# Optimization experiments

Measured on AMD Instinct MI355X. Metric: run time of the kernel, lower is better.

The kernel has to match this reference:

```python
import jax, jax.numpy as jnp
import numpy as np

B, T, N_EMBD, HEAD_SIZE = 64, 512, 384, 64


def setup_inputs() -> dict:
    key = jax.random.key(0)
    k1, k2, k3, k4 = jax.random.split(key, 4)
    x = jax.random.normal(k1, (B, T, N_EMBD), dtype=jnp.float32)
    scale = 1.0 / np.sqrt(N_EMBD)
    Wq = jax.random.normal(k2, (N_EMBD, HEAD_SIZE), dtype=jnp.float32) * scale
    Wk = jax.random.normal(k3, (N_EMBD, HEAD_SIZE), dtype=jnp.float32) * scale
    Wv = jax.random.normal(k4, (N_EMBD, HEAD_SIZE), dtype=jnp.float32) * scale
    return {"x": x, "Wq": Wq, "Wk": Wk, "Wv": Wv}


def reference(x, Wq, Wk, Wv):
    # Single-head causal self-attention (dropout = identity / eval mode).
    q = jnp.einsum('btc,ch->bth', x, Wq)  # [B,T,H]
    k = jnp.einsum('btc,ch->bth', x, Wk)
    v = jnp.einsum('btc,ch->bth', x, Wv)
    scale = q.shape[-1] ** -0.5
    scores = jnp.einsum('bth,bsh->bts', q, k) * scale  # [B,T,T]
    Tlen = x.shape[1]
    causal = jnp.tril(jnp.ones((Tlen, Tlen), dtype=bool))
    scores = jnp.where(causal, scores, -jnp.inf)
    weights = jax.nn.softmax(scores, axis=-1)
    out = jnp.einsum('bts,bsh->bth', weights, v)  # [B,T,H]
    return out
```

## Files before the change

kernel.cpp:

```cpp
#include <hip/hip_runtime.h>


typedef __bf16 bf16_t;
typedef __bf16 bf16x8 __attribute__((ext_vector_type(8)));
typedef __bf16 bf16x4 __attribute__((ext_vector_type(4)));
typedef float  f32x4  __attribute__((ext_vector_type(4)));

__device__ __forceinline__ bf16x8 ld_b128(const bf16_t* p) {
    return *reinterpret_cast<const bf16x8*>(p);
}

__device__ __forceinline__ void async_copy16(void* lds, const void* g) {
    __builtin_amdgcn_global_load_lds(
        (const __attribute__((address_space(1))) unsigned int*)g,
        (__attribute__((address_space(3))) unsigned int*)lds,
        16, 0, 0);
}

__global__ __launch_bounds__(256) void wt_kernel(const float* __restrict__ Wq,
                                                 const float* __restrict__ Wk,
                                                 const float* __restrict__ Wv,
                                                 bf16_t* __restrict__ Wt) {
    int idx = blockIdx.x * 256 + threadIdx.x;
    int p = idx / (384 * 64);
    int r = idx - p * (384 * 64);
    int c = r >> 6;
    int h = r & 63;
    const float* W = (p == 0) ? Wq : (p == 1) ? Wk : Wv;
    Wt[p * 24576 + h * 384 + c] = (bf16_t)W[c * 64 + h];
}

__global__ __launch_bounds__(256, 2) void qkv_kernel(const float* __restrict__ x,
                                                     const bf16_t* __restrict__ Wt,
                                                     bf16_t* __restrict__ Q,
                                                     bf16_t* __restrict__ K,
                                                     bf16_t* __restrict__ Vt) {
    const int tid  = threadIdx.x;
    const int wave = tid >> 6, lane = tid & 63;
    const int quad = lane >> 4, l16 = lane & 15;
    const int rowbase = blockIdx.x * 64;
    const int batch   = rowbase >> 9;

    __shared__ alignas(16) bf16_t xs[64][392];

    bf16x8 Bf[3][12];
    #pragma unroll
    for (int nt = 0; nt < 3; ++nt) {
        int col  = wave * 48 + nt * 16 + l16;
        int proj = col >> 6, h = col & 63;
        const bf16_t* wp = Wt + proj * 24576 + h * 384 + quad * 8;
        #pragma unroll
        for (int kk = 0; kk < 12; ++kk) Bf[nt][kk] = ld_b128(wp + kk * 32);
    }

    #pragma unroll
    for (int i = 0; i < 12; ++i) {
        int idx = i * 256 + tid;
        int row = idx / 48;
        int p   = idx - row * 48;
        const float* src = x + (rowbase + row) * 384 + p * 8;
        float4 a = *reinterpret_cast<const float4*>(src);
        float4 c = *reinterpret_cast<const float4*>(src + 4);
        bf16x8 v = {(bf16_t)a.x, (bf16_t)a.y, (bf16_t)a.z, (bf16_t)a.w,
                    (bf16_t)c.x, (bf16_t)c.y, (bf16_t)c.z, (bf16_t)c.w};
        *reinterpret_cast<bf16x8*>(&xs[row][p * 8]) = v;
    }
    __syncthreads();

    #pragma unroll
    for (int rt = 0; rt < 4; ++rt) {
        f32x4 acc[3];
        #pragma unroll
        for (int nt = 0; nt < 3; ++nt) acc[nt] = (f32x4){0.f, 0.f, 0.f, 0.f};

        #pragma unroll
        for (int kk = 0; kk < 12; ++kk) {
            bf16x8 a = *reinterpret_cast<const bf16x8*>(&xs[rt * 16 + l16][kk * 32 + quad * 8]);
            #pragma unroll
            for (int nt = 0; nt < 3; ++nt)
                acc[nt] = __builtin_amdgcn_mfma_f32_16x16x32_bf16(a, Bf[nt][kk], acc[nt], 0, 0, 0);
        }

        #pragma unroll
        for (int nt = 0; nt < 3; ++nt) {
            int col  = wave * 48 + nt * 16 + l16;
            int proj = col >> 6, h = col & 63;
            int trow = rowbase + rt * 16 + quad * 4;
            if (proj == 0) {
                #pragma unroll
                for (int r = 0; r < 4; ++r) Q[(trow + r) * 64 + h] = (bf16_t)acc[nt][r];
            } else if (proj == 1) {
                #pragma unroll
                for (int r = 0; r < 4; ++r) K[(trow + r) * 64 + h] = (bf16_t)acc[nt][r];
            } else {
                bf16x4 v = {(bf16_t)acc[nt][0], (bf16_t)acc[nt][1],
                            (bf16_t)acc[nt][2], (bf16_t)acc[nt][3]};
                *reinterpret_cast<bf16x4*>(Vt + batch * 32768 + h * 512 + (trow & 511)) = v;
            }
        }
    }
}

__global__ __launch_bounds__(256, 2) void attn_kernel(const bf16_t* __restrict__ Q,
                                                      const bf16_t* __restrict__ K,
                                                      const bf16_t* __restrict__ Vt,
                                                      float* __restrict__ out) {
    const int tid  = threadIdx.x;
    const int wave = tid >> 6, lane = tid & 63;
    const int quad = lane >> 4, l16 = lane & 15;
    const int b    = blockIdx.x >> 3;
    const int j    = blockIdx.x & 7;
    const int rbase = j * 64 + wave * 16;
    const int rowq  = rbase + quad * 4;

    __shared__ alignas(16) bf16_t Kt[2][64 * 64];
    __shared__ alignas(16) bf16_t Vtt[2][64 * 64];
    __shared__ alignas(16) bf16_t Pl[4][16 * 64];

    const bf16_t* Kb = K  + b * 32768;
    const bf16_t* Vb = Vt + b * 32768;

    const bf16_t* qptr = Q + (b * 512 + rbase + l16) * 64 + quad * 8;
    bf16x8 aq0 = ld_b128(qptr);
    bf16x8 aq1 = ld_b128(qptr + 32);

    f32x4 acc_o[4];
    #pragma unroll
    for (int nt = 0; nt < 4; ++nt) acc_o[nt] = (f32x4){0.f, 0.f, 0.f, 0.f};
    float l_lane[4] = {0.f, 0.f, 0.f, 0.f};

    auto stage = [&](int buf, int kb) {
        #pragma unroll
        for (int i = 0; i < 2; ++i) {
            int rr = wave * 16 + i * 8 + (lane >> 3);
            int g  = (lane & 7) ^ (rr & 7);
            async_copy16(&Kt[buf][(wave * 16 + i * 8) * 64],
                         Kb + (kb + rr) * 64 + g * 8);
            async_copy16(&Vtt[buf][(wave * 16 + i * 8) * 64],
                         Vb + rr * 512 + kb + g * 8);
        }
    };

    stage(0, 0);
    for (int kt = 0; kt <= j; ++kt) {
        int buf = kt & 1;
        __syncthreads();
        if (kt < j) stage(1 - buf, (kt + 1) * 64);
        int kb = kt * 64;
        bool last = (kt == j);

        float s[4][4];
        #pragma unroll
        for (int nt = 0; nt < 4; ++nt) {
            int tk = nt * 16 + l16;
            f32x4 c = (f32x4){0.f, 0.f, 0.f, 0.f};
            bf16x8 bk0 = ld_b128(&Kt[buf][tk * 64 + (((0 + quad) ^ (tk & 7)) << 3)]);
            c = __builtin_amdgcn_mfma_f32_16x16x32_bf16(aq0, bk0, c, 0, 0, 0);
            bf16x8 bk1 = ld_b128(&Kt[buf][tk * 64 + (((4 + quad) ^ (tk & 7)) << 3)]);
            c = __builtin_amdgcn_mfma_f32_16x16x32_bf16(aq1, bk1, c, 0, 0, 0);
            #pragma unroll
            for (int r = 0; r < 4; ++r) s[nt][r] = c[r];
        }
        if (last) {
            #pragma unroll
            for (int nt = 0; nt < 4; ++nt)
                #pragma unroll
                for (int r = 0; r < 4; ++r)
                    if (kb + nt * 16 + l16 > rowq + r) s[nt][r] = -__builtin_inff();
        }

        bf16_t* pw = &Pl[wave][0];
        #pragma unroll
        for (int nt = 0; nt < 4; ++nt) {
            #pragma unroll
            for (int r = 0; r < 4; ++r) {
                float p = __expf(fmaf(s[nt][r], 0.125f, -20.0f));
                l_lane[r] += p;
                int rl  = quad * 4 + r;
                int col = nt * 16 + l16;
                pw[rl * 64 + (((col >> 3) ^ (rl & 7)) << 3) + (col & 7)] = (bf16_t)p;
            }
        }
        bf16x8 ap0 = ld_b128(&pw[l16 * 64 + (((0 + quad) ^ (l16 & 7)) << 3)]);
        bf16x8 ap1 = ld_b128(&pw[l16 * 64 + (((4 + quad) ^ (l16 & 7)) << 3)]);
        #pragma unroll
        for (int nth = 0; nth < 4; ++nth) {
            int h = nth * 16 + l16;
            bf16x8 bv0 = ld_b128(&Vtt[buf][h * 64 + (((0 + quad) ^ (h & 7)) << 3)]);
            acc_o[nth] = __builtin_amdgcn_mfma_f32_16x16x32_bf16(ap0, bv0, acc_o[nth], 0, 0, 0);
            bf16x8 bv1 = ld_b128(&Vtt[buf][h * 64 + (((4 + quad) ^ (h & 7)) << 3)]);
            acc_o[nth] = __builtin_amdgcn_mfma_f32_16x16x32_bf16(ap1, bv1, acc_o[nth], 0, 0, 0);
        }
    }

    #pragma unroll
    for (int r = 0; r < 4; ++r) {
        float l = l_lane[r];
        #pragma unroll
        for (int xm = 1; xm < 16; xm <<= 1) l += __shfl_xor(l, xm, 64);
        l_lane[r] = l;
    }

    #pragma unroll
    for (int nth = 0; nth < 4; ++nth) {
        #pragma unroll
        for (int r = 0; r < 4; ++r) {
            out[(b * 512 + rowq + r) * 64 + nth * 16 + l16] =
                acc_o[nth][r] / l_lane[r];
        }
    }
}

extern "C" void kernel_launch(void* const* d_in, const int* in_sizes, int n_in,
                              void* d_out, int out_size, void* d_ws, size_t ws_size,
                              hipStream_t stream) {
    const float* x  = (const float*)d_in[0];
    const float* Wq = (const float*)d_in[1];
    const float* Wk = (const float*)d_in[2];
    const float* Wv = (const float*)d_in[3];

    char* ws = (char*)d_ws;
    bf16_t* Wt = (bf16_t*)(ws);
    bf16_t* Q  = (bf16_t*)(ws + 147456);
    bf16_t* K  = (bf16_t*)(ws + 147456 + 4194304);
    bf16_t* Vt = (bf16_t*)(ws + 147456 + 8388608);

    wt_kernel<<<dim3(288), dim3(256), 0, stream>>>(Wq, Wk, Wv, Wt);
    qkv_kernel<<<dim3(512), dim3(256), 0, stream>>>(x, Wt, Q, K, Vt);
    attn_kernel<<<dim3(512), dim3(256), 0, stream>>>(Q, K, Vt, (float*)d_out);
}
```

Before: 115.0 us.

## Double-buffer x tiles via async global-to-LDS loads in QKV projection

```diff
diff --git a/kernel.cpp b/kernel.cpp
--- a/kernel.cpp
+++ b/kernel.cpp
@@ -41,7 +41,7 @@
     const int rowbase = blockIdx.x * 64;
     const int batch   = rowbase >> 9;
 
-    __shared__ alignas(16) bf16_t xs[64][392];
+    __shared__ alignas(16) float xs[2][64 * 128];
 
     bf16x8 Bf[3][12];
     #pragma unroll
@@ -53,34 +53,52 @@
         for (int kk = 0; kk < 12; ++kk) Bf[nt][kk] = ld_b128(wp + kk * 32);
     }
 
-    #pragma unroll
-    for (int i = 0; i < 12; ++i) {
-        int idx = i * 256 + tid;
-        int row = idx / 48;
-        int p   = idx - row * 48;
-        const float* src = x + (rowbase + row) * 384 + p * 8;
-        float4 a = *reinterpret_cast<const float4*>(src);
-        float4 c = *reinterpret_cast<const float4*>(src + 4);
-        bf16x8 v = {(bf16_t)a.x, (bf16_t)a.y, (bf16_t)a.z, (bf16_t)a.w,
-                    (bf16_t)c.x, (bf16_t)c.y, (bf16_t)c.z, (bf16_t)c.w};
-        *reinterpret_cast<bf16x8*>(&xs[row][p * 8]) = v;
-    }
-    __syncthreads();
+    auto stage = [&](int buf, int c) {
+        const float* src = x + rowbase * 384 + c * 128;
+        #pragma unroll
+        for (int i = 0; i < 8; ++i) {
+            int g   = wave * 512 + i * 64 + lane;
+            int row = g >> 5, gc = g & 31;
+            int gs  = (gc & 24) | ((gc ^ row) & 7);
+            async_copy16(&xs[buf][(wave * 512 + i * 64) * 4],
+                         src + row * 384 + gs * 4);
+        }
+    };
+
+    f32x4 acc[4][3];
+    #pragma unroll
+    for (int rt = 0; rt < 4; ++rt)
+        #pragma unroll
+        for (int nt = 0; nt < 3; ++nt) acc[rt][nt] = (f32x4){0.f, 0.f, 0.f, 0.f};
+
+    stage(0, 0);
+    for (int c = 0; c < 3; ++c) {
+        int buf = c & 1;
+        __syncthreads();
+        if (c < 2) stage(1 - buf, c + 1);
+        #pragma unroll
+        for (int rt = 0; rt < 4; ++rt) {
+            int row = rt * 16 + l16;
+            const float* xr = &xs[buf][row * 128];
+            #pragma unroll
+            for (int kk = 0; kk < 4; ++kk) {
+                int G0 = kk * 8 + quad * 2;
+                int g0 = (G0 & 24) | ((G0 ^ row) & 7);
+                int g1 = ((G0 + 1) & 24) | (((G0 + 1) ^ row) & 7);
+                f32x4 a0 = *reinterpret_cast<const f32x4*>(xr + g0 * 4);
+                f32x4 a1 = *reinterpret_cast<const f32x4*>(xr + g1 * 4);
+                bf16x8 a = {(bf16_t)a0[0], (bf16_t)a0[1], (bf16_t)a0[2], (bf16_t)a0[3],
+                            (bf16_t)a1[0], (bf16_t)a1[1], (bf16_t)a1[2], (bf16_t)a1[3]};
+                #pragma unroll
+                for (int nt = 0; nt < 3; ++nt)
+                    acc[rt][nt] = __builtin_amdgcn_mfma_f32_16x16x32_bf16(
+                        a, Bf[nt][c * 4 + kk], acc[rt][nt], 0, 0, 0);
+            }
+        }
+    }
 
     #pragma unroll
     for (int rt = 0; rt < 4; ++rt) {
-        f32x4 acc[3];
-        #pragma unroll
-        for (int nt = 0; nt < 3; ++nt) acc[nt] = (f32x4){0.f, 0.f, 0.f, 0.f};
-
-        #pragma unroll
-        for (int kk = 0; kk < 12; ++kk) {
-            bf16x8 a = *reinterpret_cast<const bf16x8*>(&xs[rt * 16 + l16][kk * 32 + quad * 8]);
-            #pragma unroll
-            for (int nt = 0; nt < 3; ++nt)
-                acc[nt] = __builtin_amdgcn_mfma_f32_16x16x32_bf16(a, Bf[nt][kk], acc[nt], 0, 0, 0);
-        }
-
         #pragma unroll
         for (int nt = 0; nt < 3; ++nt) {
             int col  = wave * 48 + nt * 16 + l16;
@@ -88,13 +106,13 @@
             int trow = rowbase + rt * 16 + quad * 4;
             if (proj == 0) {
                 #pragma unroll
-                for (int r = 0; r < 4; ++r) Q[(trow + r) * 64 + h] = (bf16_t)acc[nt][r];
+                for (int r = 0; r < 4; ++r) Q[(trow + r) * 64 + h] = (bf16_t)acc[rt][nt][r];
             } else if (proj == 1) {
                 #pragma unroll
-                for (int r = 0; r < 4; ++r) K[(trow + r) * 64 + h] = (bf16_t)acc[nt][r];
+                for (int r = 0; r < 4; ++r) K[(trow + r) * 64 + h] = (bf16_t)acc[rt][nt][r];
             } else {
-                bf16x4 v = {(bf16_t)acc[nt][0], (bf16_t)acc[nt][1],
-                            (bf16_t)acc[nt][2], (bf16_t)acc[nt][3]};
+                bf16x4 v = {(bf16_t)acc[rt][nt][0], (bf16_t)acc[rt][nt][1],
+                            (bf16_t)acc[rt][nt][2], (bf16_t)acc[rt][nt][3]};
                 *reinterpret_cast<bf16x4*>(Vt + batch * 32768 + h * 512 + (trow & 511)) = v;
             }
         }
```

Result: no change. 117.0 us (+1.8%).
